# Kernel optimization log

Measured on AMD Instinct MI355X. Metric: run time of the kernel, lower is better.

The kernel has to match this reference:

```python
import jax, jax.numpy as jnp
import numpy as np

EPS = 1e-6
MAX_ACOSH_ARG = 1e6
MAX_DIST = 50.0
TINY = 1e-15
B, T, D = 2, 512, 512
H, N = 8, 32
A = N + 1
TAU = 1.0


def mink(x, y):
    # Lorentzian inner product over last (ambient) dim
    return -x[..., 0] * y[..., 0] + jnp.sum(x[..., 1:] * y[..., 1:], axis=-1)


def project_to_hyperboloid(x):
    xx = mink(x, x)
    scale = jnp.sqrt(jnp.maximum(jnp.abs(xx), TINY))[..., None]
    x = x / scale
    return jnp.concatenate([jnp.abs(x[..., :1]), x[..., 1:]], axis=-1)


def exp_map(p, v):
    vn = jnp.sqrt(jnp.maximum(mink(v, v), TINY))[..., None]
    y = jnp.cosh(vn) * p + (jnp.sinh(vn) / jnp.maximum(vn, TINY)) * v
    return project_to_hyperboloid(y)


def log_map(p, y):
    alpha = jnp.clip(-mink(p, y), 1.0 + EPS, MAX_ACOSH_ARG)
    dist = jnp.arccosh(alpha)[..., None]
    u = y + alpha[..., None] * p
    un = jnp.sqrt(jnp.maximum(mink(u, u), TINY))[..., None]
    return dist / jnp.maximum(un, TINY) * u


def _lift(x, W, b):
    # Linear lift -> (B,H,T,N), append time-like 0, expmap at origin
    u = (jnp.einsum('btd,dk->btk', x, W) + b).reshape(B, T, H, N).transpose(0, 2, 1, 3)
    v = jnp.concatenate([jnp.zeros(u.shape[:-1] + (1,), u.dtype), u], axis=-1)  # (B,H,T,A)
    o = jnp.zeros((A,), u.dtype).at[0].set(1.0)
    return exp_map(jnp.broadcast_to(o, v.shape), v)


def setup_inputs() -> dict:
    key = jax.random.key(0)
    ks = jax.random.split(key, 5)
    x = jax.random.normal(ks[0], (B, T, D), jnp.float32)
    Wq = jax.random.normal(ks[1], (D, H * N), jnp.float32) * 0.02
    Wk = jax.random.normal(ks[2], (D, H * N), jnp.float32) * 0.02
    Wv = jax.random.normal(ks[3], (D, H * N), jnp.float32) * 0.02
    Wo = jax.random.normal(ks[4], (H * A, D), jnp.float32) * 0.02
    return {'x': x, 'Wq': Wq, 'bq': jnp.zeros((H * N,), jnp.float32),
            'Wk': Wk, 'bk': jnp.zeros((H * N,), jnp.float32),
            'Wv': Wv, 'bv': jnp.zeros((H * N,), jnp.float32),
            'Wo': Wo, 'bo': jnp.zeros((D,), jnp.float32)}


def reference(x, Wq, bq, Wk, bk, Wv, bv, Wo, bo):
    Q = _lift(x, Wq, bq)  # (B,H,T,A) on hyperboloid
    K = _lift(x, Wk, bk)
    V = _lift(x, Wv, bv)

    # pairwise hyperbolic distances: alpha = -<q,k>_L, d = acosh(alpha)
    alpha = jnp.clip(-mink(Q[:, :, :, None, :], K[:, :, None, :, :]), 1.0 + EPS, MAX_ACOSH_ARG)
    d = jnp.minimum(jnp.arccosh(alpha), MAX_DIST)  # (B,H,T,T)
    scores = -TAU * d * d
    attn = jax.nn.softmax(scores.astype(jnp.float32), axis=-1).astype(V.dtype)

    # one Karcher step around Q
    Y = Q
    logv = log_map(Y[:, :, :, None, :], V[:, :, None, :, :])  # (B,H,T,T,A)
    step = jnp.einsum('bhqk,bhqka->bhqa', attn, logv)
    step_norm = jnp.sqrt(jnp.maximum(mink(step, step), TINY))[..., None]
    step = step * (jnp.minimum(step_norm, 20.0) / (step_norm + 1e-9))
    Y = exp_map(Y, step)  # (B,H,T,A)

    # log-map at origin anchor, project back to d_model
    o = jnp.zeros((A,), Y.dtype).at[0].set(1.0)
    Yt = Y.transpose(0, 2, 1, 3)  # (B,T,H,A)
    p0 = jnp.broadcast_to(o, Yt.shape)
    Z_tan = log_map(p0, Yt).reshape(B, T, H * A)
    Z = jnp.einsum('btk,kd->btd', Z_tan, Wo) + bo
    return Z
```

## Files before the change

### kernel.cpp

```cpp
#include <hip/hip_runtime.h>
#include <math.h>

#define EPSF 1e-6f
#define MAX_ACOSH_ARGF 1e6f
#define MAX_DISTF 50.0f
#define TINYF 1e-15f

typedef float f4v __attribute__((ext_vector_type(4)));
typedef float f2v __attribute__((ext_vector_type(2)));

constexpr int OFF_U  = 0;
constexpr int OFF_OP = 0;
constexpr int OFF_ZT = 1048576;
constexpr int OFF_Q  = 3145728;
constexpr int OFF_KT = 3440640;
constexpr int OFF_VT = 3735552;

__device__ __forceinline__ float facosh(float a) {
    return __logf(a + sqrtf((a - 1.0f) * (a + 1.0f)));
}

__global__ __launch_bounds__(256, 4) void qkv_gemm(
    const float* __restrict__ x,
    const float* __restrict__ Wq, const float* __restrict__ Wk,
    const float* __restrict__ Wv, float* __restrict__ U)
{
    const int tid  = threadIdx.x;
    const int wid  = tid >> 6;
    const int lane = tid & 63;
    const int blk  = blockIdx.x;
    const int rt   = blk & 63;
    const int cs   = blk >> 6;
    const int ct   = cs % 6;
    const int s    = cs / 6;
    const int m0   = rt * 16 + wid * 4;
    const int tsel = ct >> 1;
    const int n0t  = (ct & 1) * 128;
    const float* W = (tsel == 0) ? Wq : (tsel == 1) ? Wk : Wv;
    const int c0   = n0t + lane * 2;
    const int k0   = s * 128;
    const float* xb = x + m0 * 512 + k0;
    const float* wp = W + k0 * 256 + c0;

    float acc[4][2];
    #pragma unroll
    for (int r = 0; r < 4; ++r) { acc[r][0] = 0.0f; acc[r][1] = 0.0f; }

    f4v a[2][4][2];
    f2v b[2][8];

#define LDQ(B, KB)                                                      \
    { _Pragma("unroll") for (int r = 0; r < 4; ++r) {                   \
          a[B][r][0] = *(const f4v*)(xb + r * 512 + (KB));              \
          a[B][r][1] = *(const f4v*)(xb + r * 512 + (KB) + 4); }        \
      _Pragma("unroll") for (int j = 0; j < 8; ++j)                     \
          b[B][j] = *(const f2v*)(wp + ((KB) + j) * 256); }
#define STQ(B)                                                          \
    { _Pragma("unroll") for (int j = 0; j < 8; ++j) {                   \
        _Pragma("unroll") for (int r = 0; r < 4; ++r) {                 \
            const float av = a[B][r][j >> 2][j & 3];                    \
            acc[r][0] = fmaf(av, b[B][j][0], acc[r][0]);                \
            acc[r][1] = fmaf(av, b[B][j][1], acc[r][1]); } } }

    LDQ(0, 0) LDQ(1, 8)
    for (int kb = 0; kb < 112; kb += 16) {
        STQ(0) LDQ(0, kb + 16)
        STQ(1) LDQ(1, kb + 24)
    }
    STQ(0) STQ(1)
#undef LDQ
#undef STQ

    #pragma unroll
    for (int r = 0; r < 4; ++r)
        *(f2v*)(U + (s * 1024 + m0 + r) * 768 + tsel * 256 + c0) =
            f2v{acc[r][0], acc[r][1]};
}

__global__ __launch_bounds__(768) void lift_kernel(
    const float* __restrict__ U,
    const float* __restrict__ bq, const float* __restrict__ bk,
    const float* __restrict__ bv,
    float* __restrict__ Qp, float* __restrict__ KT, float* __restrict__ VT)
{
    const int bt = blockIdx.x;
    const int b  = bt >> 9, t = bt & 511;
    const int j  = threadIdx.x;
    const int tsel = j >> 8, h = (j >> 5) & 7, cin = j & 31;

    const float* bias = (tsel == 0) ? bq : (tsel == 1) ? bk : bv;
    float u = bias[j & 255];
    #pragma unroll
    for (int s = 0; s < 4; ++s) u += U[s * 786432 + bt * 768 + j];

    float n2 = u * u;
    #pragma unroll
    for (int msk = 1; msk < 32; msk <<= 1) n2 += __shfl_xor(n2, msk, 64);
    n2 = fmaxf(n2, TINYF);
    const float vn = sqrtf(n2);
    const float ch = coshf(vn);
    const float sh = sinhf(vn) / fmaxf(vn, TINYF);
    const float xx = fmaf(sh * sh, n2, -ch * ch);
    const float scale = sqrtf(fmaxf(fabsf(xx), TINYF));
    const float fs = sh / scale;
    const float tc = fabsf(ch / scale);
    const int bh = b * 8 + h;

    if (tsel == 0) {
        float* qp = Qp + (bh * 512 + t) * 36;
        qp[1 + cin] = fs * u;
        if (cin == 0) { qp[0] = tc; qp[33] = 0.0f; qp[34] = 0.0f; qp[35] = 0.0f; }
    } else {
        float* P = ((tsel == 1) ? KT : VT) + bh * 18432;
        const int a0 = 1 + cin;
        P[(a0 >> 2) * 2048 + t * 4 + (a0 & 3)] = fs * u;
        if (cin == 0) {
            P[t * 4] = tc;
            P[8 * 2048 + t * 4 + 1] = 0.0f;
            P[8 * 2048 + t * 4 + 2] = 0.0f;
            P[8 * 2048 + t * 4 + 3] = 0.0f;
        }
    }
}

__global__ __launch_bounds__(256) void attn_kernel(
    const float* __restrict__ Qp, const float* __restrict__ KT,
    const float* __restrict__ VT, float* __restrict__ ZT)
{
    __shared__ float part[2][4][34];

    const int tid   = threadIdx.x;
    const int blk   = blockIdx.x;
    const int bh    = blk >> 6;
    const int q0    = (blk & 63) * 8;
    const int wid   = tid >> 6;
    const int lane  = tid & 63;
    const int g     = lane >> 4;
    const int t     = lane & 15;
    const int quad  = wid >> 1;
    const int khalf = wid & 1;
    const int qi    = q0 + quad * 4 + g;

    float qn[36];
    {
        const float* qp = Qp + (bh * 512 + qi) * 36;
        #pragma unroll
        for (int jj = 0; jj < 9; ++jj) {
            const f4v v = *(const f4v*)(qp + 4 * jj);
            #pragma unroll
            for (int i = 0; i < 4; ++i) {
                const int a = 4 * jj + i;
                qn[a] = (a == 0) ? v[i] : -v[i];
            }
        }
    }

    const f4v* K4 = (const f4v*)KT + bh * 4608;
    const f4v* V4 = (const f4v*)VT + bh * 4608;

    float l = 0.0f;
    float ac[33];
    #pragma unroll
    for (int a = 0; a < 33; ++a) ac[a] = 0.0f;

    for (int st = 0; st < 16; ++st) {
        const int k = t + 16 * st + 256 * khalf;
        f4v kr[9], vr[9];
        #pragma unroll
        for (int jj = 0; jj < 9; ++jj) kr[jj] = K4[jj * 512 + k];
        #pragma unroll
        for (int jj = 0; jj < 9; ++jj) vr[jj] = V4[jj * 512 + k];

        float p0 = 0.f, p1 = 0.f, p2 = 0.f, p3 = 0.f;
        #pragma unroll
        for (int jj = 0; jj < 9; ++jj) {
            p0 = fmaf(qn[4 * jj],     kr[jj][0], p0);
            p1 = fmaf(qn[4 * jj + 1], kr[jj][1], p1);
            p2 = fmaf(qn[4 * jj + 2], kr[jj][2], p2);
            p3 = fmaf(qn[4 * jj + 3], kr[jj][3], p3);
        }
        const float a1 = (p0 + p1) + (p2 + p3);

        float r0 = 0.f, r1 = 0.f, r2 = 0.f, r3 = 0.f;
        #pragma unroll
        for (int jj = 0; jj < 9; ++jj) {
            r0 = fmaf(qn[4 * jj],     vr[jj][0], r0);
            r1 = fmaf(qn[4 * jj + 1], vr[jj][1], r1);
            r2 = fmaf(qn[4 * jj + 2], vr[jj][2], r2);
            r3 = fmaf(qn[4 * jj + 3], vr[jj][3], r3);
        }
        const float a2 = (r0 + r1) + (r2 + r3);

        const float a1c = fminf(fmaxf(a1, 1.0f + EPSF), MAX_ACOSH_ARGF);
        const float dd  = fminf(facosh(a1c), MAX_DISTF);
        const float e   = __expf(-dd * dd);
        const float a2c = fminf(fmaxf(a2, 1.0f + EPSF), MAX_ACOSH_ARGF);
        const float w   = e * facosh(a2c);
        l += e;
        #pragma unroll
        for (int a = 0; a < 33; ++a) ac[a] = fmaf(w, vr[a >> 2][a & 3], ac[a]);
    }

    #pragma unroll
    for (int msk = 1; msk < 16; msk <<= 1) l += __shfl_xor(l, msk, 64);
    #pragma unroll
    for (int a = 0; a < 33; ++a) {
        float v = ac[a];
        #pragma unroll
        for (int msk = 1; msk < 16; msk <<= 1) v += __shfl_xor(v, msk, 64);
        ac[a] = v;
    }

    if (khalf == 1 && t == 0) {
        part[quad][g][0] = l;
        #pragma unroll
        for (int a = 0; a < 33; ++a) part[quad][g][1 + a] = ac[a];
    }
    __syncthreads();
    if (khalf == 1) return;

    l += part[quad][g][0];
    #pragma unroll
    for (int a = 0; a < 33; ++a) ac[a] += part[quad][g][1 + a];

    float sw = 0.0f;
    #pragma unroll
    for (int a = 0; a < 33; ++a) sw = fmaf(qn[a], ac[a], sw);
    const float un_c   = 3.1622776601683794e-8f;
    const float inv_un = (1.0f / l) / un_c;
    ac[0] = fmaf(sw, qn[0], ac[0]) * inv_un;
    #pragma unroll
    for (int a = 1; a < 33; ++a) ac[a] = fmaf(-sw, qn[a], ac[a]) * inv_un;

    float mk = -ac[0] * ac[0];
    #pragma unroll
    for (int a = 1; a < 33; ++a) mk = fmaf(ac[a], ac[a], mk);
    const float snorm = sqrtf(fmaxf(mk, TINYF));
    const float fac   = fminf(snorm, 20.0f) / (snorm + 1e-9f);
    #pragma unroll
    for (int a = 0; a < 33; ++a) ac[a] *= fac;

    float mk2 = -ac[0] * ac[0];
    #pragma unroll
    for (int a = 1; a < 33; ++a) mk2 = fmaf(ac[a], ac[a], mk2);
    const float vn  = sqrtf(fmaxf(mk2, TINYF));
    const float ch  = coshf(vn);
    const float shr = sinhf(vn) / fmaxf(vn, TINYF);
    ac[0] = fmaf(ch, qn[0], shr * ac[0]);
    #pragma unroll
    for (int a = 1; a < 33; ++a) ac[a] = fmaf(-ch, qn[a], shr * ac[a]);

    float xx = -ac[0] * ac[0];
    #pragma unroll
    for (int a = 1; a < 33; ++a) xx = fmaf(ac[a], ac[a], xx);
    const float scale = sqrtf(fmaxf(fabsf(xx), TINYF));

    const float Y0  = fabsf(ac[0] / scale);
    const float al3 = fminf(fmaxf(Y0, 1.0f + EPSF), MAX_ACOSH_ARGF);
    const float d3  = acoshf(al3);
    const float f3  = d3 / un_c;

    if (t == 0) {
        const int b = bh >> 3, h = bh & 7;
        float* zp = ZT + (b * 512 + qi) * 264 + h * 33;
        zp[0] = f3 * (Y0 + al3);
        const float fsc = f3 / scale;
        #pragma unroll
        for (int a = 1; a < 33; ++a) zp[a] = fsc * ac[a];
    }
}

__global__ __launch_bounds__(256, 4) void out_gemm(
    const float* __restrict__ ZT, const float* __restrict__ Wo,
    float* __restrict__ OP)
{
    const int tid  = threadIdx.x;
    const int wid  = tid >> 6;
    const int lane = tid & 63;
    const int blk  = blockIdx.x;
    const int rt   = blk & 63;
    const int cs   = blk >> 6;
    const int ct   = cs & 7;
    const int s    = cs >> 3;
    const int m0   = rt * 16 + wid * 4;
    const int c0   = ct * 64 + lane;
    const int k0   = s * 132;
    const float* zb = ZT + m0 * 264 + k0;
    const float* wp = Wo + k0 * 512 + c0;

    float acc[4] = {0.f, 0.f, 0.f, 0.f};
    f4v a[2][4];
    float bv[2][4];

#define LDO(B, KK)                                                      \
    { _Pragma("unroll") for (int r = 0; r < 4; ++r)                     \
          a[B][r] = *(const f4v*)(zb + r * 264 + (KK));                 \
      _Pragma("unroll") for (int jj = 0; jj < 4; ++jj)                  \
          bv[B][jj] = wp[((KK) + jj) * 512]; }
#define STO(B)                                                          \
    { _Pragma("unroll") for (int jj = 0; jj < 4; ++jj) {                \
        _Pragma("unroll") for (int r = 0; r < 4; ++r)                   \
            acc[r] = fmaf(a[B][r][jj], bv[B][jj], acc[r]); } }

    LDO(0, 0) LDO(1, 4)
    for (int kb = 0; kb < 120; kb += 8) {
        STO(0) LDO(0, kb + 8)
        STO(1) LDO(1, kb + 12)
    }
    STO(0) LDO(0, 128)
    STO(1)
    STO(0)
#undef LDO
#undef STO

    #pragma unroll
    for (int r = 0; r < 4; ++r)
        OP[s * 524288 + (m0 + r) * 512 + c0] = acc[r];
}

__global__ __launch_bounds__(256) void out_reduce(
    const float* __restrict__ OP, const float* __restrict__ bo,
    float* __restrict__ out)
{
    const int i4 = blockIdx.x * 256 + threadIdx.x;
    const f4v p0 = ((const f4v*)OP)[i4];
    const f4v p1 = ((const f4v*)OP)[i4 + 131072];
    const f4v bb = ((const f4v*)bo)[i4 & 127];
    ((f4v*)out)[i4] = p0 + p1 + bb;
}

extern "C" void kernel_launch(void* const* d_in, const int* in_sizes, int n_in,
                              void* d_out, int out_size, void* d_ws, size_t ws_size,
                              hipStream_t stream) {
    const float* x  = (const float*)d_in[0];
    const float* Wq = (const float*)d_in[1];
    const float* bq = (const float*)d_in[2];
    const float* Wk = (const float*)d_in[3];
    const float* bk = (const float*)d_in[4];
    const float* Wv = (const float*)d_in[5];
    const float* bv = (const float*)d_in[6];
    const float* Wo = (const float*)d_in[7];
    const float* bo = (const float*)d_in[8];
    float* out = (float*)d_out;
    float* ws  = (float*)d_ws;

    float* U   = ws + OFF_U;
    float* OP  = ws + OFF_OP;
    float* ZTp = ws + OFF_ZT;
    float* Qp  = ws + OFF_Q;
    float* KT  = ws + OFF_KT;
    float* VT  = ws + OFF_VT;

    qkv_gemm<<<1536, 256, 0, stream>>>(x, Wq, Wk, Wv, U);
    lift_kernel<<<1024, 768, 0, stream>>>(U, bq, bk, bv, Qp, KT, VT);
    attn_kernel<<<1024, 256, 0, stream>>>(Qp, KT, VT, ZTp);
    out_gemm<<<1024, 256, 0, stream>>>(ZTp, Wo, OP);
    out_reduce<<<512, 256, 0, stream>>>(OP, bo, out);
}
```

Before: 203.6 us.

## Store K/V row-major, use packed FMA, drop key-split reduction in attention

The lift kernel now writes K and V in the same 36-float per-token row layout as Q, instead of a transposed structure-of-arrays layout. The attention kernel has each wave loop over all 512 keys for its 4 queries, which removes the two-wave key split, the shared-memory partial exchange and the __syncthreads. The dot products and the accumulation are rewritten with float4 elementwise FMA so the compiler can emit packed FP32 FMAs. The grid is halved to 512 blocks, so there are fewer waves to hide latency, and per-lane K/V loads are now strided by row instead of coalesced across lanes.

```diff
diff --git a/kernel.cpp b/kernel.cpp
--- a/kernel.cpp
+++ b/kernel.cpp
@@ -13,8 +13,8 @@
 constexpr int OFF_OP = 0;
 constexpr int OFF_ZT = 1048576;
 constexpr int OFF_Q  = 3145728;
-constexpr int OFF_KT = 3440640;
-constexpr int OFF_VT = 3735552;
+constexpr int OFF_K  = 3440640;
+constexpr int OFF_V  = 3735552;
 
 __device__ __forceinline__ float facosh(float a) {
     return __logf(a + sqrtf((a - 1.0f) * (a + 1.0f)));
@@ -81,7 +81,7 @@
     const float* __restrict__ U,
     const float* __restrict__ bq, const float* __restrict__ bk,
     const float* __restrict__ bv,
-    float* __restrict__ Qp, float* __restrict__ KT, float* __restrict__ VT)
+    float* __restrict__ Qp, float* __restrict__ Kp, float* __restrict__ Vp)
 {
     const int bt = blockIdx.x;
     const int b  = bt >> 9, t = bt & 511;
@@ -106,90 +106,63 @@
     const float tc = fabsf(ch / scale);
     const int bh = b * 8 + h;
 
-    if (tsel == 0) {
-        float* qp = Qp + (bh * 512 + t) * 36;
-        qp[1 + cin] = fs * u;
-        if (cin == 0) { qp[0] = tc; qp[33] = 0.0f; qp[34] = 0.0f; qp[35] = 0.0f; }
-    } else {
-        float* P = ((tsel == 1) ? KT : VT) + bh * 18432;
-        const int a0 = 1 + cin;
-        P[(a0 >> 2) * 2048 + t * 4 + (a0 & 3)] = fs * u;
-        if (cin == 0) {
-            P[t * 4] = tc;
-            P[8 * 2048 + t * 4 + 1] = 0.0f;
-            P[8 * 2048 + t * 4 + 2] = 0.0f;
-            P[8 * 2048 + t * 4 + 3] = 0.0f;
-        }
+    float* P = ((tsel == 0) ? Qp : (tsel == 1) ? Kp : Vp) + (bh * 512 + t) * 36;
+    P[1 + cin] = fs * u;
+    if (cin == 0) {
+        P[0] = tc;
+        P[33] = 0.0f; P[34] = 0.0f; P[35] = 0.0f;
     }
 }
 
 __global__ __launch_bounds__(256) void attn_kernel(
-    const float* __restrict__ Qp, const float* __restrict__ KT,
-    const float* __restrict__ VT, float* __restrict__ ZT)
-{
-    __shared__ float part[2][4][34];
-
-    const int tid   = threadIdx.x;
-    const int blk   = blockIdx.x;
-    const int bh    = blk >> 6;
-    const int q0    = (blk & 63) * 8;
-    const int wid   = tid >> 6;
-    const int lane  = tid & 63;
-    const int g     = lane >> 4;
-    const int t     = lane & 15;
-    const int quad  = wid >> 1;
-    const int khalf = wid & 1;
-    const int qi    = q0 + quad * 4 + g;
-
-    float qn[36];
+    const float* __restrict__ Qp, const float* __restrict__ Kp,
+    const float* __restrict__ Vp, float* __restrict__ ZT)
+{
+    const int tid  = threadIdx.x;
+    const int blk  = blockIdx.x;
+    const int bh   = blk >> 5;
+    const int q0   = (blk & 31) * 16;
+    const int wid  = tid >> 6;
+    const int lane = tid & 63;
+    const int g    = lane >> 4;
+    const int t    = lane & 15;
+    const int qi   = q0 + wid * 4 + g;
+
+    f4v qn4[9];
     {
         const float* qp = Qp + (bh * 512 + qi) * 36;
         #pragma unroll
-        for (int jj = 0; jj < 9; ++jj) {
-            const f4v v = *(const f4v*)(qp + 4 * jj);
-            #pragma unroll
-            for (int i = 0; i < 4; ++i) {
-                const int a = 4 * jj + i;
-                qn[a] = (a == 0) ? v[i] : -v[i];
-            }
+        for (int j = 0; j < 9; ++j) {
+            const f4v v = *(const f4v*)(qp + 4 * j);
+            qn4[j] = f4v{(j == 0) ? v[0] : -v[0], -v[1], -v[2], -v[3]};
         }
     }
 
-    const f4v* K4 = (const f4v*)KT + bh * 4608;
-    const f4v* V4 = (const f4v*)VT + bh * 4608;
+    const float* kp = Kp + (bh * 512 + t) * 36;
+    const float* vp = Vp + (bh * 512 + t) * 36;
 
     float l = 0.0f;
-    float ac[33];
-    #pragma unroll
-    for (int a = 0; a < 33; ++a) ac[a] = 0.0f;
-
-    for (int st = 0; st < 16; ++st) {
-        const int k = t + 16 * st + 256 * khalf;
+    f4v acv[9];
+    #pragma unroll
+    for (int j = 0; j < 9; ++j) acv[j] = f4v{0.f, 0.f, 0.f, 0.f};
+
+    for (int st = 0; st < 32; ++st) {
         f4v kr[9], vr[9];
         #pragma unroll
-        for (int jj = 0; jj < 9; ++jj) kr[jj] = K4[jj * 512 + k];
-        #pragma unroll
-        for (int jj = 0; jj < 9; ++jj) vr[jj] = V4[jj * 512 + k];
-
-        float p0 = 0.f, p1 = 0.f, p2 = 0.f, p3 = 0.f;
-        #pragma unroll
-        for (int jj = 0; jj < 9; ++jj) {
-            p0 = fmaf(qn[4 * jj],     kr[jj][0], p0);
-            p1 = fmaf(qn[4 * jj + 1], kr[jj][1], p1);
-            p2 = fmaf(qn[4 * jj + 2], kr[jj][2], p2);
-            p3 = fmaf(qn[4 * jj + 3], kr[jj][3], p3);
-        }
-        const float a1 = (p0 + p1) + (p2 + p3);
-
-        float r0 = 0.f, r1 = 0.f, r2 = 0.f, r3 = 0.f;
-        #pragma unroll
-        for (int jj = 0; jj < 9; ++jj) {
-            r0 = fmaf(qn[4 * jj],     vr[jj][0], r0);
-            r1 = fmaf(qn[4 * jj + 1], vr[jj][1], r1);
-            r2 = fmaf(qn[4 * jj + 2], vr[jj][2], r2);
-            r3 = fmaf(qn[4 * jj + 3], vr[jj][3], r3);
-        }
-        const float a2 = (r0 + r1) + (r2 + r3);
+        for (int j = 0; j < 9; ++j) kr[j] = *(const f4v*)(kp + 4 * j);
+        #pragma unroll
+        for (int j = 0; j < 9; ++j) vr[j] = *(const f4v*)(vp + 4 * j);
+        kp += 16 * 36; vp += 16 * 36;
+
+        f4v p4 = qn4[0] * kr[0];
+        #pragma unroll
+        for (int j = 1; j < 9; ++j) p4 = __builtin_elementwise_fma(qn4[j], kr[j], p4);
+        const float a1 = (p4[0] + p4[1]) + (p4[2] + p4[3]);
+
+        f4v r4 = qn4[0] * vr[0];
+        #pragma unroll
+        for (int j = 1; j < 9; ++j) r4 = __builtin_elementwise_fma(qn4[j], vr[j], r4);
+        const float a2 = (r4[0] + r4[1]) + (r4[2] + r4[3]);
 
         const float a1c = fminf(fmaxf(a1, 1.0f + EPSF), MAX_ACOSH_ARGF);
         const float dd  = fminf(facosh(a1c), MAX_DISTF);
@@ -197,31 +170,30 @@
         const float a2c = fminf(fmaxf(a2, 1.0f + EPSF), MAX_ACOSH_ARGF);
         const float w   = e * facosh(a2c);
         l += e;
-        #pragma unroll
-        for (int a = 0; a < 33; ++a) ac[a] = fmaf(w, vr[a >> 2][a & 3], ac[a]);
+        const f4v w4 = f4v{w, w, w, w};
+        #pragma unroll
+        for (int j = 0; j < 9; ++j) acv[j] = __builtin_elementwise_fma(w4, vr[j], acv[j]);
     }
 
     #pragma unroll
     for (int msk = 1; msk < 16; msk <<= 1) l += __shfl_xor(l, msk, 64);
     #pragma unroll
+    for (int j = 0; j < 9; ++j) {
+        #pragma unroll
+        for (int i = 0; i < 4; ++i) {
+            float v = acv[j][i];
+            #pragma unroll
+            for (int msk = 1; msk < 16; msk <<= 1) v += __shfl_xor(v, msk, 64);
+            acv[j][i] = v;
+        }
+    }
+
+    float ac[33], qn[33];
+    #pragma unroll
     for (int a = 0; a < 33; ++a) {
-        float v = ac[a];
-        #pragma unroll
-        for (int msk = 1; msk < 16; msk <<= 1) v += __shfl_xor(v, msk, 64);
-        ac[a] = v;
-    }
-
-    if (khalf == 1 && t == 0) {
-        part[quad][g][0] = l;
-        #pragma unroll
-        for (int a = 0; a < 33; ++a) part[quad][g][1 + a] = ac[a];
-    }
-    __syncthreads();
-    if (khalf == 1) return;
-
-    l += part[quad][g][0];
-    #pragma unroll
-    for (int a = 0; a < 33; ++a) ac[a] += part[quad][g][1 + a];
+        ac[a] = acv[a >> 2][a & 3];
+        qn[a] = qn4[a >> 2][a & 3];
+    }
 
     float sw = 0.0f;
     #pragma unroll
@@ -348,12 +320,12 @@
     float* OP  = ws + OFF_OP;
     float* ZTp = ws + OFF_ZT;
     float* Qp  = ws + OFF_Q;
-    float* KT  = ws + OFF_KT;
-    float* VT  = ws + OFF_VT;
+    float* Kp  = ws + OFF_K;
+    float* Vp  = ws + OFF_V;
 
     qkv_gemm<<<1536, 256, 0, stream>>>(x, Wq, Wk, Wv, U);
-    lift_kernel<<<1024, 768, 0, stream>>>(U, bq, bk, bv, Qp, KT, VT);
-    attn_kernel<<<1024, 256, 0, stream>>>(Qp, KT, VT, ZTp);
+    lift_kernel<<<1024, 768, 0, stream>>>(U, bq, bk, bv, Qp, Kp, Vp);
+    attn_kernel<<<512, 256, 0, stream>>>(Qp, Kp, Vp, ZTp);
     out_gemm<<<1024, 256, 0, stream>>>(ZTp, Wo, OP);
     out_reduce<<<512, 256, 0, stream>>>(OP, bo, out);
 }
```

After: 218.8 us. +7.4%, slower.
